# Kernel optimization log

Hardware: AMD Instinct MI355X
Metric: run time of the kernel (lower is better)

Reference implementation:

```python
import jax, jax.numpy as jnp
import numpy as np

N_GAUSSIANS = 512
N_PIXELS = 262144  # 512x512 image


def setup_inputs() -> dict:
    key = jax.random.key(0)
    k1, k2, k3, k4, k5 = jax.random.split(key, 5)
    x = jax.random.uniform(k1, (N_PIXELS, 2), dtype=jnp.float32)
    alphas = (1.0 / N_GAUSSIANS) ** 0.5 * jax.random.uniform(k2, (N_GAUSSIANS, 1), dtype=jnp.float32)
    means = jax.random.uniform(k3, (N_GAUSSIANS, 2), dtype=jnp.float32)
    rotations = jnp.pi * jax.random.uniform(k4, (N_GAUSSIANS, 1), dtype=jnp.float32)
    scales = 0.1 * jax.random.uniform(k5, (N_GAUSSIANS, 2), dtype=jnp.float32)
    return {"x": x, "alphas": alphas, "means": means, "rotations": rotations, "scales": scales}


def _inv2x2(m):
    # m: [N, 2, 2] -> elementwise 2x2 inverse
    a, b = m[:, 0, 0], m[:, 0, 1]
    c, d = m[:, 1, 0], m[:, 1, 1]
    det = a * d - b * c
    inv = jnp.stack([jnp.stack([d, -b], axis=-1),
                     jnp.stack([-c, a], axis=-1)], axis=-2)
    return inv / det[:, None, None]


def reference(x, alphas, means, rotations, scales):
    rot = rotations[:, 0]                       # [N]
    cth, sth = jnp.cos(rot), jnp.sin(rot)
    s0, s1 = scales[:, 0], scales[:, 1]
    # RS = R @ diag(s): [N, 2, 2]
    RS = jnp.stack([s0 * cth, -s1 * sth, s0 * sth, s1 * cth], axis=-1).reshape(-1, 2, 2)
    RSSR = jnp.einsum('nij,nkj->nik', RS, RS)   # RS @ RS^T
    cov = _inv2x2(RSSR)                          # [N, 2, 2]
    rel = x[:, None, :] - means[None, :, :]      # [P, N, 2]
    q = jnp.einsum('pni,nij,pnj->pn', rel, cov, rel)  # quadratic form [P, N]
    g = jnp.exp(-q / 2)                          # [P, N]
    return g @ alphas                            # [P, 1]
```

## Files before the change

### kernel.cpp

```cpp
#include <hip/hip_runtime.h>

#define NG 512
#define NPX 262144
#define GRID1D 32
#define NCELL 1024
#define NSEG 32
#define SEGCAP 32
#define PXCAP 384
#define KSCALE 0.72134752044448170368f
#define WCULL 30.0f


__global__ __launch_bounds__(256)
void prep_kernel(const float* __restrict__ alphas,
                 const float* __restrict__ means,
                 const float* __restrict__ rotations,
                 const float* __restrict__ scales,
                 float4* __restrict__ pg, float4* __restrict__ cg)
{
    int n = blockIdx.x * 256 + threadIdx.x;
    if (n >= NG) return;
    float rot = rotations[n];
    float sth, cth;
    sincosf(rot, &sth, &cth);
    float s0 = scales[2 * n + 0];
    float s1 = scales[2 * n + 1];
    float r00 = s0 * cth, r01 = -s1 * sth;
    float r10 = s0 * sth, r11 =  s1 * cth;
    float Ar = r00 * r00 + r01 * r01;
    float Br = r00 * r10 + r01 * r11;
    float Dr = r10 * r10 + r11 * r11;
    float det = Ar * Dr - Br * Br;
    float kc00 =  KSCALE * Dr / det;
    float kc01 = -KSCALE * Br / det;
    float p00 = sqrtf(kc00);
    float p01 = kc01 / p00;
    float p11 = sqrtf(KSCALE / Dr);
    float mx = means[2 * n + 0];
    float my = means[2 * n + 1];
    float nu  = -(p00 * mx + p01 * my);
    float nv  = -(p11 * my);
    float l2a = log2f(alphas[n]);

    pg[2 * n + 0] = make_float4(p00, p01, nu, l2a);
    pg[2 * n + 1] = make_float4(p11, nv, 0.0f, 0.0f);

    float r2 = l2a + WCULL;
    float hx = -1.0f, hy = -1.0f;
    if (r2 > 0.0f) {
        float rk = r2 * (1.0f / KSCALE);
        hx = sqrtf(rk * Ar);
        hy = sqrtf(rk * Dr);
    }
    cg[n] = make_float4(mx, my, hx, hy);
}

__global__ __launch_bounds__(256)
void bin_kernel(const float* __restrict__ x, int* __restrict__ cur,
                float4* __restrict__ entries)
{
    int t = blockIdx.x * 256 + threadIdx.x;
    float4 p2 = ((const float4*)x)[t];
    int seg = blockIdx.x & (NSEG - 1);

    int cxa = min((int)(p2.x * GRID1D), GRID1D - 1);
    int cya = min((int)(p2.y * GRID1D), GRID1D - 1);
    int ca  = cya * GRID1D + cxa;
    int cxb = min((int)(p2.z * GRID1D), GRID1D - 1);
    int cyb = min((int)(p2.w * GRID1D), GRID1D - 1);
    int cb  = cyb * GRID1D + cxb;

    int pa = atomicAdd(&cur[seg * NCELL + ca], 1);
    int pb = atomicAdd(&cur[seg * NCELL + cb], 1);
    if (pa < SEGCAP)
        entries[(seg * NCELL + ca) * SEGCAP + pa] =
            make_float4(p2.x, p2.y, __int_as_float(2 * t), 0.0f);
    if (pb < SEGCAP)
        entries[(seg * NCELL + cb) * SEGCAP + pb] =
            make_float4(p2.z, p2.w, __int_as_float(2 * t + 1), 0.0f);
}

__global__ __launch_bounds__(128, 2)
void splat_kernel(const int* __restrict__ cur,
                  const float4* __restrict__ entries,
                  const float4* __restrict__ pg,
                  const float4* __restrict__ cg,
                  float* __restrict__ out)
{
    __shared__ float4 gl[2 * (NG + 4)];
    __shared__ float2 px[PXCAP];
    __shared__ int    pidx[PXCAP];
    __shared__ int    cnt[NSEG], preS[NSEG];
    __shared__ int    nkept, totsh;

    int tid  = threadIdx.x;
    int cell = blockIdx.x;

    if (tid == 0) nkept = 0;
    if (tid < NSEG) cnt[tid] = min(cur[tid * NCELL + cell], SEGCAP);
    __syncthreads();

    if (tid < 64) {
        int v = (tid < NSEG) ? cnt[tid] : 0;
        #pragma unroll
        for (int d = 1; d < NSEG; d <<= 1) {
            int w = __shfl_up(v, d, 64);
            if (tid >= d) v += w;
        }
        if (tid < NSEG) preS[tid] = v - cnt[tid];
        if (tid == NSEG - 1) totsh = min(v, PXCAP);
    }
    __syncthreads();
    int total = totsh;

    #pragma unroll
    for (int slot = 0; slot < NSEG * SEGCAP; slot += 128) {
        int sl = slot + tid;
        int s = sl >> 5;
        int k = sl & (SEGCAP - 1);
        if (k < cnt[s]) {
            int dst = preS[s] + k;
            if (dst < PXCAP) {
                float4 e = entries[(s * NCELL + cell) * SEGCAP + k];
                px[dst]   = make_float2(e.x, e.y);
                pidx[dst] = __float_as_int(e.z);
            }
        }
    }

    float ccx = ((cell & (GRID1D - 1)) + 0.5f) * (1.0f / GRID1D);
    float ccy = ((cell >> 5)           + 0.5f) * (1.0f / GRID1D);
    const float HW = 0.5f / GRID1D;
    for (int n = tid; n < NG; n += 128) {
        float4 c = cg[n];
        if (fabsf(c.x - ccx) <= c.z + HW && fabsf(c.y - ccy) <= c.w + HW) {
            int slot = atomicAdd(&nkept, 1);
            gl[2 * slot + 0] = pg[2 * n + 0];
            gl[2 * slot + 1] = pg[2 * n + 1];
        }
    }
    __syncthreads();

    int nk = nkept;
    int nround = (nk + 3) & ~3;
    if (tid < nround - nk) {
        gl[2 * (nk + tid) + 0] = make_float4(0.0f, 0.0f, 0.0f, -10000.0f);
        gl[2 * (nk + tid) + 1] = make_float4(0.0f, 0.0f, 0.0f, 0.0f);
    }
    __syncthreads();

    for (int p0 = tid; 2 * p0 < total; p0 += 128) {
        int ia = 2 * p0, ib = ia + 1;
        bool hasB = ib < total;
        float2 A = px[ia];
        float2 B = hasB ? px[ib] : A;
        float a0 = 0.0f, a1 = 0.0f, b0 = 0.0f, b1 = 0.0f;

        for (int j = 0; j < nround; j += 4) {
            #pragma unroll
            for (int jj = 0; jj < 4; ++jj) {
                float4 P = gl[2 * (j + jj) + 0];
                float4 Q = gl[2 * (j + jj) + 1];
                float uA = fmaf(P.x, A.x, fmaf(P.y, A.y, P.z));
                float vA = fmaf(Q.x, A.y, Q.y);
                float wA = fmaf(-vA, vA, fmaf(-uA, uA, P.w));
                float uB = fmaf(P.x, B.x, fmaf(P.y, B.y, P.z));
                float vB = fmaf(Q.x, B.y, Q.y);
                float wB = fmaf(-vB, vB, fmaf(-uB, uB, P.w));
                float eA = __builtin_amdgcn_exp2f(wA);
                float eB = __builtin_amdgcn_exp2f(wB);
                if (jj & 1) { a1 += eA; b1 += eB; }
                else        { a0 += eA; b0 += eB; }
            }
        }

        out[pidx[ia]] = a0 + a1;
        if (hasB) out[pidx[ib]] = b0 + b1;
    }
}

extern "C" void kernel_launch(void* const* d_in, const int* in_sizes, int n_in,
                              void* d_out, int out_size, void* d_ws, size_t ws_size,
                              hipStream_t stream) {
    const float* x         = (const float*)d_in[0];
    const float* alphas    = (const float*)d_in[1];
    const float* means     = (const float*)d_in[2];
    const float* rotations = (const float*)d_in[3];
    const float* scales    = (const float*)d_in[4];
    float* out = (float*)d_out;

    char* ws = (char*)d_ws;
    size_t off = 0;
    int*    cur     = (int*)(ws + off);    off += (size_t)NSEG * NCELL * sizeof(int);
    float4* entries = (float4*)(ws + off); off += (size_t)NSEG * NCELL * SEGCAP * sizeof(float4);
    float4* pg      = (float4*)(ws + off); off += (size_t)NG * 2 * sizeof(float4);
    float4* cg      = (float4*)(ws + off);

    hipMemsetAsync(cur, 0, NSEG * NCELL * sizeof(int), stream);
    prep_kernel<<<(NG + 255) / 256, 256, 0, stream>>>(alphas, means, rotations, scales, pg, cg);
    bin_kernel<<<NPX / 512, 256, 0, stream>>>(x, cur, entries);
    splat_kernel<<<NCELL, 128, 0, stream>>>(cur, entries, pg, cg, out);
}
```

Measured before the change: 108.1 us.

## Split per-cell Gaussian culling into separate kernel and read culled list from global

Moves per-cell Gaussian culling into a new cull_kernel that writes a compacted per-cell parameter list to global memory. The splat kernel then reads Gaussian parameters straight from global memory (uniform across lanes, so served from cache) instead of staging about 16KB in LDS. This frees LDS so the launch bound can rise to 4 blocks per SM. Bin entries shrink from float4 to a pixel index, and the splat kernel gathers coordinates from x. The cost is an extra launch, global writes of up to 1024×16KB, and the risk that global or scalar loads in the inner loop are slower than LDS reads.

```diff
diff --git a/kernel.cpp b/kernel.cpp
--- a/kernel.cpp
+++ b/kernel.cpp
@@ -7,6 +7,7 @@
 #define NSEG 32
 #define SEGCAP 32
 #define PXCAP 384
+#define CLCAP 512
 #define KSCALE 0.72134752044448170368f
 #define WCULL 30.0f
 
@@ -57,7 +58,7 @@
 
 __global__ __launch_bounds__(256)
 void bin_kernel(const float* __restrict__ x, int* __restrict__ cur,
-                float4* __restrict__ entries)
+                int* __restrict__ entries)
 {
     int t = blockIdx.x * 256 + threadIdx.x;
     float4 p2 = ((const float4*)x)[t];
@@ -72,31 +73,59 @@
 
     int pa = atomicAdd(&cur[seg * NCELL + ca], 1);
     int pb = atomicAdd(&cur[seg * NCELL + cb], 1);
-    if (pa < SEGCAP)
-        entries[(seg * NCELL + ca) * SEGCAP + pa] =
-            make_float4(p2.x, p2.y, __int_as_float(2 * t), 0.0f);
-    if (pb < SEGCAP)
-        entries[(seg * NCELL + cb) * SEGCAP + pb] =
-            make_float4(p2.z, p2.w, __int_as_float(2 * t + 1), 0.0f);
-}
-
-__global__ __launch_bounds__(128, 2)
+    if (pa < SEGCAP) entries[(seg * NCELL + ca) * SEGCAP + pa] = 2 * t;
+    if (pb < SEGCAP) entries[(seg * NCELL + cb) * SEGCAP + pb] = 2 * t + 1;
+}
+
+__global__ __launch_bounds__(128)
+void cull_kernel(const float4* __restrict__ pg, const float4* __restrict__ cg,
+                 float4* __restrict__ cl, int* __restrict__ gcount)
+{
+    __shared__ int nkept;
+    int tid = threadIdx.x, cell = blockIdx.x;
+    if (tid == 0) nkept = 0;
+    __syncthreads();
+
+    float ccx = ((cell & (GRID1D - 1)) + 0.5f) * (1.0f / GRID1D);
+    float ccy = ((cell >> 5)           + 0.5f) * (1.0f / GRID1D);
+    const float HW = 0.5f / GRID1D;
+    float4* base = cl + (size_t)cell * 2 * CLCAP;
+
+    for (int n = tid; n < NG; n += 128) {
+        float4 c = cg[n];
+        if (fabsf(c.x - ccx) <= c.z + HW && fabsf(c.y - ccy) <= c.w + HW) {
+            int s = atomicAdd(&nkept, 1);
+            base[2 * s + 0] = pg[2 * n + 0];
+            base[2 * s + 1] = pg[2 * n + 1];
+        }
+    }
+    __syncthreads();
+
+    int nk = nkept;
+    int nr = (nk + 3) & ~3;
+    if (tid < nr - nk) {
+        base[2 * (nk + tid) + 0] = make_float4(0.0f, 0.0f, 0.0f, -10000.0f);
+        base[2 * (nk + tid) + 1] = make_float4(0.0f, 0.0f, 0.0f, 0.0f);
+    }
+    if (tid == 0) gcount[cell] = nr;
+}
+
+__global__ __launch_bounds__(128, 4)
 void splat_kernel(const int* __restrict__ cur,
-                  const float4* __restrict__ entries,
-                  const float4* __restrict__ pg,
-                  const float4* __restrict__ cg,
+                  const int* __restrict__ entries,
+                  const float* __restrict__ x,
+                  const float4* __restrict__ cl,
+                  const int* __restrict__ gcount,
                   float* __restrict__ out)
 {
-    __shared__ float4 gl[2 * (NG + 4)];
     __shared__ float2 px[PXCAP];
     __shared__ int    pidx[PXCAP];
     __shared__ int    cnt[NSEG], preS[NSEG];
-    __shared__ int    nkept, totsh;
+    __shared__ int    totsh;
 
     int tid  = threadIdx.x;
     int cell = blockIdx.x;
 
-    if (tid == 0) nkept = 0;
     if (tid < NSEG) cnt[tid] = min(cur[tid * NCELL + cell], SEGCAP);
     __syncthreads();
 
@@ -112,6 +141,7 @@
     }
     __syncthreads();
     int total = totsh;
+    if (total == 0) return;
 
     #pragma unroll
     for (int slot = 0; slot < NSEG * SEGCAP; slot += 128) {
@@ -121,33 +151,16 @@
         if (k < cnt[s]) {
             int dst = preS[s] + k;
             if (dst < PXCAP) {
-                float4 e = entries[(s * NCELL + cell) * SEGCAP + k];
-                px[dst]   = make_float2(e.x, e.y);
-                pidx[dst] = __float_as_int(e.z);
+                int id = entries[(s * NCELL + cell) * SEGCAP + k];
+                px[dst]   = ((const float2*)x)[id];
+                pidx[dst] = id;
             }
         }
     }
-
-    float ccx = ((cell & (GRID1D - 1)) + 0.5f) * (1.0f / GRID1D);
-    float ccy = ((cell >> 5)           + 0.5f) * (1.0f / GRID1D);
-    const float HW = 0.5f / GRID1D;
-    for (int n = tid; n < NG; n += 128) {
-        float4 c = cg[n];
-        if (fabsf(c.x - ccx) <= c.z + HW && fabsf(c.y - ccy) <= c.w + HW) {
-            int slot = atomicAdd(&nkept, 1);
-            gl[2 * slot + 0] = pg[2 * n + 0];
-            gl[2 * slot + 1] = pg[2 * n + 1];
-        }
-    }
-    __syncthreads();
-
-    int nk = nkept;
-    int nround = (nk + 3) & ~3;
-    if (tid < nround - nk) {
-        gl[2 * (nk + tid) + 0] = make_float4(0.0f, 0.0f, 0.0f, -10000.0f);
-        gl[2 * (nk + tid) + 1] = make_float4(0.0f, 0.0f, 0.0f, 0.0f);
-    }
-    __syncthreads();
+    __syncthreads();
+
+    int ng = gcount[cell];
+    const float4* base = cl + (size_t)cell * 2 * CLCAP;
 
     for (int p0 = tid; 2 * p0 < total; p0 += 128) {
         int ia = 2 * p0, ib = ia + 1;
@@ -156,11 +169,11 @@
         float2 B = hasB ? px[ib] : A;
         float a0 = 0.0f, a1 = 0.0f, b0 = 0.0f, b1 = 0.0f;
 
-        for (int j = 0; j < nround; j += 4) {
+        for (int j = 0; j < ng; j += 4) {
             #pragma unroll
             for (int jj = 0; jj < 4; ++jj) {
-                float4 P = gl[2 * (j + jj) + 0];
-                float4 Q = gl[2 * (j + jj) + 1];
+                float4 P = base[2 * (j + jj) + 0];
+                float4 Q = base[2 * (j + jj) + 1];
                 float uA = fmaf(P.x, A.x, fmaf(P.y, A.y, P.z));
                 float vA = fmaf(Q.x, A.y, Q.y);
                 float wA = fmaf(-vA, vA, fmaf(-uA, uA, P.w));
@@ -192,12 +205,15 @@
     char* ws = (char*)d_ws;
     size_t off = 0;
     int*    cur     = (int*)(ws + off);    off += (size_t)NSEG * NCELL * sizeof(int);
-    float4* entries = (float4*)(ws + off); off += (size_t)NSEG * NCELL * SEGCAP * sizeof(float4);
+    int*    entries = (int*)(ws + off);    off += (size_t)NSEG * NCELL * SEGCAP * sizeof(int);
     float4* pg      = (float4*)(ws + off); off += (size_t)NG * 2 * sizeof(float4);
-    float4* cg      = (float4*)(ws + off);
+    float4* cg      = (float4*)(ws + off); off += (size_t)NG * sizeof(float4);
+    int*    gcount  = (int*)(ws + off);    off += (size_t)NCELL * sizeof(int);
+    float4* cl      = (float4*)(ws + off);
 
     hipMemsetAsync(cur, 0, NSEG * NCELL * sizeof(int), stream);
     prep_kernel<<<(NG + 255) / 256, 256, 0, stream>>>(alphas, means, rotations, scales, pg, cg);
     bin_kernel<<<NPX / 512, 256, 0, stream>>>(x, cur, entries);
-    splat_kernel<<<NCELL, 128, 0, stream>>>(cur, entries, pg, cg, out);
-}
+    cull_kernel<<<NCELL, 128, 0, stream>>>(pg, cg, cl, gcount);
+    splat_kernel<<<NCELL, 128, 0, stream>>>(cur, entries, x, cl, gcount, out);
+}
```

After: 138.7 us. 1.28x slower.
